# Kernel tuning notes

Measured on AMD Instinct MI355X. Metric: run time of the kernel, lower is better.

The kernel has to match this reference:

```python
import jax, jax.numpy as jnp
import numpy as np

LN_EPS = 1e-5   # torch nn.LayerNorm default
R_EPS = 1e-8    # eps used in log(R.clamp(min=eps))


def layernorm(x, g, b):
    mu = jnp.mean(x, axis=-1, keepdims=True)
    var = jnp.var(x, axis=-1, keepdims=True)
    return (x - mu) * jax.lax.rsqrt(var + LN_EPS) * g + b


def setup_inputs() -> dict:
    S, B, C, h, w, d = 4, 1, 128, 10, 10, 10
    nL = 2  # num_layers
    key = jax.random.key(0)
    ks = jax.random.split(key, 20)
    std = 0.02
    inp = {
        "z": jax.random.normal(ks[0], (S, B, C, h, w, d), jnp.float32),
        "r": jax.random.uniform(ks[1], (S,), jnp.float32, 0.1, 1.0),
        "seq_embed": std * jax.random.normal(ks[2], (S, C), jnp.float32),
        # per-layer attention params, stacked on leading layer axis
        "Wq": std * jax.random.normal(ks[3], (nL, C, C), jnp.float32),
        "Wk": std * jax.random.normal(ks[4], (nL, C, C), jnp.float32),
        "Wv": std * jax.random.normal(ks[5], (nL, C, C), jnp.float32),
        "Wp": std * jax.random.normal(ks[6], (nL, C, C), jnp.float32),
        "beta": jnp.ones((nL,), jnp.float32),
        "ln1_g": jnp.ones((nL, C), jnp.float32),
        "ln1_b": jnp.zeros((nL, C), jnp.float32),
        # FFN params
        "ffn_w1": std * jax.random.normal(ks[7], (C, 4 * C), jnp.float32),
        "ffn_b1": jnp.zeros((4 * C,), jnp.float32),
        "ffn_w2": std * jax.random.normal(ks[8], (4 * C, C), jnp.float32),
        "ffn_b2": jnp.zeros((C,), jnp.float32),
        "ln2_g": jnp.ones((C,), jnp.float32),
        "ln2_b": jnp.zeros((C,), jnp.float32),
    }
    return inp


def _forward(z, r, seq_embed, Wq, Wk, Wv, Wp, beta, ln1_g, ln1_b,
             ffn_w1, ffn_b1, ffn_w2, ffn_b2, ln2_g, ln2_b):
    S, B, C, h, w, d = z.shape
    N = h * w * d
    L = S * N
    nL, _, _ = Wq.shape
    H = 8
    Dh = C // H
    scale = Dh ** (-0.5)

    # tokenize: [S,B,C,h,w,d] -> [B, S*N, C] with per-sequence embedding added
    tokens = z.reshape(S, B, C, N).transpose(1, 0, 3, 2)      # [B,S,N,C]
    tokens = tokens + seq_embed[None, :, None, :]
    tokens = tokens.reshape(B, L, C)

    # reliability bias: log(clamp(outer(r_tok, r_tok), eps))  [L,L]
    r_tok = jnp.repeat(r, N)                                   # [L]
    log_R = jnp.log(jnp.clip(r_tok[:, None] * r_tok[None, :], R_EPS, None))

    for l in range(nL):
        residual = tokens
        Q = (tokens @ Wq[l]).reshape(B, L, H, Dh)
        K = (tokens @ Wk[l]).reshape(B, L, H, Dh)
        V = (tokens @ Wv[l]).reshape(B, L, H, Dh)
        attn = jnp.einsum('bihd,bjhd->bhij', Q, K) * scale     # [B,H,L,L]
        attn = attn + beta[l] * log_R[None, None]
        attn = jax.nn.softmax(attn, axis=-1)
        out = jnp.einsum('bhij,bjhd->bihd', attn, V).reshape(B, L, C)
        out = out @ Wp[l]
        tokens = layernorm(out + residual, ln1_g[l], ln1_b[l])

    # FFN (exact GELU, matching torch nn.GELU default) + residual + LN
    hdn = jax.nn.gelu(tokens @ ffn_w1 + ffn_b1, approximate=False)
    tokens = layernorm((hdn @ ffn_w2 + ffn_b2) + tokens, ln2_g, ln2_b)

    # de-tokenize: [B,L,C] -> [B, S*C, h, w, d]
    tokens = tokens.reshape(B, S, N, C).transpose(0, 1, 3, 2)  # [B,S,C,N]
    return tokens.reshape(B, S * C, h, w, d)


def reference(z, r, seq_embed, Wq, Wk, Wv, Wp, beta, ln1_g, ln1_b,
              ffn_w1, ffn_b1, ffn_w2, ffn_b2, ln2_g, ln2_b):
    return _forward(z, r, seq_embed, Wq, Wk, Wv, Wp, beta, ln1_g, ln1_b,
                    ffn_w1, ffn_b1, ffn_w2, ffn_b2, ln2_g, ln2_b)
```

## Files before the change

### kernel.cpp

```cpp
#include <hip/hip_runtime.h>
#include <hip/hip_bf16.h>
#include <math.h>

#define LL 4000
#define CC 128
#define NN 1000
#define NLAYER 2
#define KSPLIT 4
#define SCLOG2 0.36067376022224085f
#define KROW 20
#define VROW 36

typedef __attribute__((ext_vector_type(4))) short bf16x4;
typedef __attribute__((ext_vector_type(8))) short short8;
typedef __attribute__((ext_vector_type(4))) float f32x4;
typedef __attribute__((ext_vector_type(2))) unsigned int u32x2;

__device__ __forceinline__ short bf16rne(float f) {
    return __builtin_bit_cast(short, __float2bfloat16(f));
}
__device__ __forceinline__ float bf16tof(short s) {
    return __builtin_bit_cast(float, (unsigned)((unsigned short)s) << 16);
}

__device__ __forceinline__ bf16x4 pack4(const float* p) {
    unsigned w01 = __builtin_amdgcn_perm(__builtin_bit_cast(unsigned, p[1]),
                                         __builtin_bit_cast(unsigned, p[0]),
                                         0x07060302u);
    unsigned w23 = __builtin_amdgcn_perm(__builtin_bit_cast(unsigned, p[3]),
                                         __builtin_bit_cast(unsigned, p[2]),
                                         0x07060302u);
    u32x2 w = {w01, w23};
    return __builtin_bit_cast(bf16x4, w);
}

__global__ void tokenize_kernel(const float* __restrict__ z,
                                const float* __restrict__ se,
                                float* __restrict__ tok,
                                short* __restrict__ tokb) {
    __shared__ float tl[32][33];
    const int s  = blockIdx.z;
    const int c0 = blockIdx.y * 32;
    const int n0 = blockIdx.x * 32;
    const int tx = threadIdx.x & 31, ty = threadIdx.x >> 5;
    #pragma unroll
    for (int i = 0; i < 4; ++i) {
        int n = n0 + tx;
        if (n < NN) tl[ty * 4 + i][tx] = z[((size_t)s * CC + c0 + ty * 4 + i) * NN + n];
    }
    __syncthreads();
    #pragma unroll
    for (int i = 0; i < 4; ++i) {
        int n = n0 + ty * 4 + i;
        if (n < NN) {
            int c = c0 + tx;
            float v = tl[tx][ty * 4 + i] + se[s * CC + c];
            size_t o = ((size_t)(s * NN + n)) * CC + c;
            tok[o] = v;
            tokb[o] = bf16rne(v);
        }
    }
}

__global__ void detok_kernel(const float* __restrict__ tok,
                             float* __restrict__ out) {
    __shared__ float tl[32][33];
    const int s  = blockIdx.z;
    const int c0 = blockIdx.y * 32;
    const int n0 = blockIdx.x * 32;
    const int tx = threadIdx.x & 31, ty = threadIdx.x >> 5;
    #pragma unroll
    for (int i = 0; i < 4; ++i) {
        int n = n0 + ty * 4 + i;
        if (n < NN) tl[ty * 4 + i][tx] = tok[((size_t)(s * NN + n)) * CC + c0 + tx];
    }
    __syncthreads();
    #pragma unroll
    for (int i = 0; i < 4; ++i) {
        int n = n0 + tx;
        if (n < NN) out[((size_t)s * CC + c0 + ty * 4 + i) * NN + n] = tl[tx][ty * 4 + i];
    }
}

__global__ void prep_weights(const float* __restrict__ Wq, const float* __restrict__ Wk,
                             const float* __restrict__ Wv, const float* __restrict__ Wp,
                             const float* __restrict__ w1, const float* __restrict__ w2,
                             const float* __restrict__ r, const float* __restrict__ beta,
                             short* __restrict__ wt8, short* __restrict__ w1t,
                             short* __restrict__ w2t, float* __restrict__ kbw) {
    int idx = blockIdx.x * blockDim.x + threadIdx.x;
    if (idx < 8 * 16384) {
        int m = idx >> 14, i = idx & 16383;
        int n = i >> 7, k = i & 127;
        const float* src = (m < 2) ? Wq + (size_t)m * 16384
                         : (m < 4) ? Wk + (size_t)(m - 2) * 16384
                         : (m < 6) ? Wv + (size_t)(m - 4) * 16384
                                   : Wp + (size_t)(m - 6) * 16384;
        wt8[idx] = bf16rne(src[k * 128 + n]);
    } else if (idx < 8 * 16384 + 65536) {
        int i = idx - 8 * 16384;
        int n = i >> 7, k = i & 127;
        w1t[i] = bf16rne(w1[(size_t)k * 512 + n]);
    } else if (idx < 8 * 16384 + 2 * 65536) {
        int i = idx - 8 * 16384 - 65536;
        int n = i >> 9, k = i & 511;
        w2t[i] = bf16rne(w2[(size_t)k * 128 + n]);
    } else if (idx < 8 * 16384 + 2 * 65536 + NLAYER * KSPLIT) {
        int i = idx - (8 * 16384 + 2 * 65536);
        int l = i / KSPLIT, zz = i - l * KSPLIT;
        kbw[i] = exp2f(beta[l] * __log2f(r[zz]));
    }
}

__device__ __forceinline__ void gemm_body(
        const short* __restrict__ A, const short* __restrict__ Wt,
        const float* __restrict__ bias, void* __restrict__ outp,
        int M, int K, int N, int flags, int row0, int col0) {
    __shared__ short Al[16][136];
    __shared__ short Wl[128][136];
    const int tid = threadIdx.x;
    const int lane = tid & 63;
    const int w = tid >> 6;
    const int lq = lane & 15, g = lane >> 4;

    f32x4 acc[2] = {{0.f,0.f,0.f,0.f},{0.f,0.f,0.f,0.f}};

    for (int kc = 0; kc < K; kc += 128) {
        {
            int r = tid >> 4, c = (tid & 15) * 8;
            *(short8*)&Al[r][c] = *(const short8*)(A + (size_t)(row0 + r) * K + kc + c);
        }
        {
            int c = (tid & 15) * 8;
            int nb = tid >> 4;
            #pragma unroll
            for (int i = 0; i < 8; ++i) {
                int n = nb + i * 16;
                *(short8*)&Wl[n][c] = *(const short8*)(Wt + (size_t)(col0 + n) * K + kc + c);
            }
        }
        __syncthreads();
        bf16x4 af[8];
        #pragma unroll
        for (int ks = 0; ks < 8; ++ks)
            af[ks] = *(const bf16x4*)&Al[lq][ks * 16 + g * 4];
        #pragma unroll
        for (int ct = 0; ct < 2; ++ct) {
            int n = (w * 2 + ct) * 16 + lq;
            #pragma unroll
            for (int ks = 0; ks < 8; ++ks) {
                bf16x4 bfr = *(const bf16x4*)&Wl[n][ks * 16 + g * 4];
                acc[ct] = __builtin_amdgcn_mfma_f32_16x16x16bf16_1k(af[ks], bfr, acc[ct], 0, 0, 0);
            }
        }
        __syncthreads();
    }
    #pragma unroll
    for (int ct = 0; ct < 2; ++ct) {
        int col = col0 + (w * 2 + ct) * 16 + lq;
        float bv = bias ? bias[col] : 0.f;
        float v[4];
        #pragma unroll
        for (int r = 0; r < 4; ++r) {
            v[r] = acc[ct][r] + bv;
            if (flags & 2) v[r] = 0.5f * v[r] * (1.f + erff(v[r] * 0.70710678118654752f));
            if (flags & 8) v[r] *= SCLOG2;
        }
        if (flags & 4) {
            bf16x4 res = {bf16rne(v[0]), bf16rne(v[1]), bf16rne(v[2]), bf16rne(v[3])};
            *(bf16x4*)((short*)outp + (size_t)col * M + row0 + g * 4) = res;
        } else if (flags & 16) {
            #pragma unroll
            for (int r = 0; r < 4; ++r)
                ((short*)outp)[((size_t)(col >> 4) * M + (row0 + g * 4 + r)) * 16 + (col & 15)] = bf16rne(v[r]);
        } else if (flags & 1) {
            #pragma unroll
            for (int r = 0; r < 4; ++r)
                ((short*)outp)[(size_t)(row0 + g * 4 + r) * N + col] = bf16rne(v[r]);
        } else {
            #pragma unroll
            for (int r = 0; r < 4; ++r)
                ((float*)outp)[(size_t)(row0 + g * 4 + r) * N + col] = v[r];
        }
    }
}

__global__ __launch_bounds__(256) void mfma_gemm(
        const short* __restrict__ A, const short* __restrict__ Wt,
        const float* __restrict__ bias, void* __restrict__ outp,
        int M, int K, int N, int flags) {
    gemm_body(A, Wt, bias, outp, M, K, N, flags,
              blockIdx.x * 16, blockIdx.y * 128);
}

__global__ __launch_bounds__(256) void mfma_gemm3(
        const short* __restrict__ A,
        const short* __restrict__ W0, const short* __restrict__ W1,
        const short* __restrict__ W2,
        short* __restrict__ o0, short* __restrict__ o1, short* __restrict__ o2,
        int M, int K, int N) {
    const short* Wt = (blockIdx.z == 0) ? W0 : (blockIdx.z == 1) ? W1 : W2;
    short* o = (blockIdx.z == 0) ? o0 : (blockIdx.z == 1) ? o1 : o2;
    int flags = (blockIdx.z == 0) ? (1 | 8) : (blockIdx.z == 1) ? 16 : 4;
    gemm_body(A, Wt, nullptr, o, M, K, N, flags, blockIdx.x * 16, 0);
}

__global__ __launch_bounds__(256) void mfma_gemm_ln(
        const short* __restrict__ A, const short* __restrict__ Wt,
        const float* __restrict__ bias, const float* __restrict__ resid,
        const float* __restrict__ gam, const float* __restrict__ bet,
        float* __restrict__ outf, short* __restrict__ outb,
        int M, int K) {
    __shared__ short Al[16][136];
    __shared__ short Wl[128][136];
    __shared__ float sL[4][4][4], s2L[4][4][4];
    const int tid = threadIdx.x;
    const int lane = tid & 63;
    const int w = tid >> 6;
    const int lq = lane & 15, g = lane >> 4;
    const int row0 = blockIdx.x * 16;

    f32x4 acc[2] = {{0.f,0.f,0.f,0.f},{0.f,0.f,0.f,0.f}};

    for (int kc = 0; kc < K; kc += 128) {
        {
            int r = tid >> 4, c = (tid & 15) * 8;
            *(short8*)&Al[r][c] = *(const short8*)(A + (size_t)(row0 + r) * K + kc + c);
        }
        {
            int c = (tid & 15) * 8;
            int nb = tid >> 4;
            #pragma unroll
            for (int i = 0; i < 8; ++i) {
                int n = nb + i * 16;
                *(short8*)&Wl[n][c] = *(const short8*)(Wt + (size_t)n * K + kc + c);
            }
        }
        __syncthreads();
        bf16x4 af[8];
        #pragma unroll
        for (int ks = 0; ks < 8; ++ks)
            af[ks] = *(const bf16x4*)&Al[lq][ks * 16 + g * 4];
        #pragma unroll
        for (int ct = 0; ct < 2; ++ct) {
            int n = (w * 2 + ct) * 16 + lq;
            #pragma unroll
            for (int ks = 0; ks < 8; ++ks) {
                bf16x4 bfr = *(const bf16x4*)&Wl[n][ks * 16 + g * 4];
                acc[ct] = __builtin_amdgcn_mfma_f32_16x16x16bf16_1k(af[ks], bfr, acc[ct], 0, 0, 0);
            }
        }
        __syncthreads();
    }

    float v[2][4];
    int cols[2] = {(w * 2) * 16 + lq, (w * 2 + 1) * 16 + lq};
    #pragma unroll
    for (int ct = 0; ct < 2; ++ct) {
        float bv = bias ? bias[cols[ct]] : 0.f;
        #pragma unroll
        for (int r = 0; r < 4; ++r)
            v[ct][r] = acc[ct][r] + bv +
                       resid[(size_t)(row0 + g * 4 + r) * CC + cols[ct]];
    }
    float sr[4], s2r[4];
    #pragma unroll
    for (int r = 0; r < 4; ++r) {
        sr[r]  = v[0][r] + v[1][r];
        s2r[r] = v[0][r] * v[0][r] + v[1][r] * v[1][r];
    }
    #pragma unroll
    for (int off = 1; off < 16; off <<= 1) {
        #pragma unroll
        for (int r = 0; r < 4; ++r) {
            sr[r]  += __shfl_xor(sr[r],  off);
            s2r[r] += __shfl_xor(s2r[r], off);
        }
    }
    if (lq == 0) {
        #pragma unroll
        for (int r = 0; r < 4; ++r) { sL[w][g][r] = sr[r]; s2L[w][g][r] = s2r[r]; }
    }
    __syncthreads();
    #pragma unroll
    for (int r = 0; r < 4; ++r) {
        float s = 0.f, s2 = 0.f;
        #pragma unroll
        for (int ww = 0; ww < 4; ++ww) { s += sL[ww][g][r]; s2 += s2L[ww][g][r]; }
        float mu = s * (1.f / CC);
        float var = s2 * (1.f / CC) - mu * mu;
        float rstd = rsqrtf(var + 1e-5f);
        size_t rowoff = (size_t)(row0 + g * 4 + r) * CC;
        #pragma unroll
        for (int ct = 0; ct < 2; ++ct) {
            float y = (v[ct][r] - mu) * rstd * gam[cols[ct]] + bet[cols[ct]];
            outf[rowoff + cols[ct]] = y;
            outb[rowoff + cols[ct]] = bf16rne(y);
        }
    }
}

__global__ __launch_bounds__(256) void attn_mfma_kernel(
        const short* __restrict__ Qb, const short* __restrict__ Kh,
        const short* __restrict__ Vt, const float* __restrict__ kbw,
        short* __restrict__ pob, float* __restrict__ pl) {
    __shared__ short Kl[2][32][KROW];
    __shared__ short Vl[2][16][VROW];
    const int tid  = threadIdx.x;
    const int lane = tid & 63;
    const int wv   = tid >> 6;
    const int lq = lane & 15;
    const int g  = lane >> 4;
    const int h  = blockIdx.y;
    const int z  = blockIdx.z;
    const int qt = blockIdx.x * 4 + wv;
    const int q0 = qt * 16;
    const int hd0 = h * 16;
    const int kbase = z * NN;
    const bool qvalid = qt < LL / 16;

    bf16x4 qf = {0, 0, 0, 0};
    if (qvalid) qf = *(const bf16x4*)(Qb + (size_t)(q0 + lq) * CC + hd0 + 4 * g);

    const short onev = (lq == 0) ? (short)0x3F80 : (short)0;
    const bf16x4 af1 = {onev, onev, onev, onev};

    const short* kgp = Kh + ((size_t)h * LL + kbase) * 16 + tid * 2;
    const short* vgp = Vt + (size_t)(hd0 + (tid >> 4)) * LL + kbase + (tid & 15) * 2;
    short* kwp = &Kl[0][0][0] + (tid >> 3) * KROW + (tid & 7) * 2;
    short* vwp = &Vl[0][0][0] + (tid >> 4) * VROW + (tid & 15) * 2;
    const int kbufstride = 32 * KROW;
    const int vbufstride = 16 * VROW;

    f32x4 o  = {0.f, 0.f, 0.f, 0.f};
    f32x4 ps = {0.f, 0.f, 0.f, 0.f};

    {
        unsigned kd = *(const unsigned*)kgp;
        unsigned vd = *(const unsigned*)vgp;
        *(unsigned*)kwp = kd;
        *(unsigned*)vwp = vd;
    }
    unsigned kdA = *(const unsigned*)(kgp + (size_t)32 * 16);
    unsigned vdA = *(const unsigned*)(vgp + 32);
    __syncthreads();

    for (int t = 0; t < 31; ++t) {
        unsigned kdB, vdB;
        if (t < 30) {
            kdB = *(const unsigned*)(kgp + (size_t)(t + 2) * 32 * 16);
            vdB = *(const unsigned*)(vgp + (t + 2) * 32);
        }

        {
            const short* kb = &Kl[t & 1][0][0];
            const short* vb = &Vl[t & 1][0][0];
            bf16x4 K0 = *(const bf16x4*)(kb + lq * KROW + 4 * g);
            bf16x4 K1 = *(const bf16x4*)(kb + (16 + lq) * KROW + 4 * g);
            bf16x4 V0 = *(const bf16x4*)(vb + lq * VROW + 4 * g);
            bf16x4 V1 = *(const bf16x4*)(vb + lq * VROW + 16 + 4 * g);
            const f32x4 zz = {0.f, 0.f, 0.f, 0.f};
            f32x4 s0 = __builtin_amdgcn_mfma_f32_16x16x16bf16_1k(K0, qf, zz, 0, 0, 0);
            f32x4 s1 = __builtin_amdgcn_mfma_f32_16x16x16bf16_1k(K1, qf, zz, 0, 0, 0);
            float p0[4], p1[4];
            #pragma unroll
            for (int r = 0; r < 4; ++r) {
                p0[r] = __builtin_amdgcn_exp2f(s0[r]);
                p1[r] = __builtin_amdgcn_exp2f(s1[r]);
            }
            bf16x4 pt0 = pack4(p0);
            bf16x4 pt1 = pack4(p1);
            o  = __builtin_amdgcn_mfma_f32_16x16x16bf16_1k(V0, pt0, o, 0, 0, 0);
            o  = __builtin_amdgcn_mfma_f32_16x16x16bf16_1k(V1, pt1, o, 0, 0, 0);
            ps = __builtin_amdgcn_mfma_f32_16x16x16bf16_1k(af1, pt0, ps, 0, 0, 0);
            ps = __builtin_amdgcn_mfma_f32_16x16x16bf16_1k(af1, pt1, ps, 0, 0, 0);
        }

        const int nb = (t + 1) & 1;
        *(unsigned*)(kwp + nb * kbufstride) = kdA;
        *(unsigned*)(vwp + nb * vbufstride) = vdA;
        __syncthreads();
        if (t < 30) { kdA = kdB; vdA = vdB; }
    }

    {
        const short* kb = &Kl[1][0][0];
        const short* vb = &Vl[1][0][0];
        bf16x4 K0 = *(const bf16x4*)(kb + lq * KROW + 4 * g);
        bf16x4 V0 = *(const bf16x4*)(vb + lq * VROW + 4 * g);
        if (g >= 2) V0 = (bf16x4){0, 0, 0, 0};
        const f32x4 zz = {0.f, 0.f, 0.f, 0.f};
        f32x4 s0 = __builtin_amdgcn_mfma_f32_16x16x16bf16_1k(K0, qf, zz, 0, 0, 0);
        float p0[4];
        #pragma unroll
        for (int r = 0; r < 4; ++r)
            p0[r] = (g < 2) ? __builtin_amdgcn_exp2f(s0[r]) : 0.f;
        bf16x4 pt0 = pack4(p0);
        o  = __builtin_amdgcn_mfma_f32_16x16x16bf16_1k(V0, pt0, o, 0, 0, 0);
        ps = __builtin_amdgcn_mfma_f32_16x16x16bf16_1k(af1, pt0, ps, 0, 0, 0);
    }

    if (qvalid) {
        const float wz = kbw[z];
        bf16x4 ow = {bf16rne(o[0] * wz), bf16rne(o[1] * wz),
                     bf16rne(o[2] * wz), bf16rne(o[3] * wz)};
        *(bf16x4*)(pob + (size_t)z * LL * CC + (size_t)(q0 + lq) * CC + hd0 + 4 * g) = ow;
        if (g == 0) pl[(z * 8 + h) * LL + q0 + lq] = ps[0] * wz;
    }
}

__global__ void attn_combine(const short* __restrict__ pob,
                             const float* __restrict__ pl,
                             short* __restrict__ attb) {
    int i = blockIdx.x * blockDim.x + threadIdx.x;
    if (i >= LL * CC / 4) return;
    int q  = i >> 5;
    int c0 = (i & 31) * 4;
    int h  = c0 >> 4;
    size_t off = (size_t)q * CC + c0;
    float o0 = 0.f, o1 = 0.f, o2 = 0.f, o3 = 0.f;
    float l = 0.f;
    #pragma unroll
    for (int zz = 0; zz < KSPLIT; ++zz) {
        bf16x4 t = *(const bf16x4*)(pob + (size_t)zz * LL * CC + off);
        o0 += bf16tof(t[0]); o1 += bf16tof(t[1]);
        o2 += bf16tof(t[2]); o3 += bf16tof(t[3]);
        l += pl[(zz * 8 + h) * LL + q];
    }
    float inv = 1.f / l;
    bf16x4 res = {bf16rne(o0 * inv), bf16rne(o1 * inv),
                  bf16rne(o2 * inv), bf16rne(o3 * inv)};
    *(bf16x4*)(attb + off) = res;
}

extern "C" void kernel_launch(void* const* d_in, const int* in_sizes, int n_in,
                              void* d_out, int out_size, void* d_ws, size_t ws_size,
                              hipStream_t stream) {
    const float* z    = (const float*)d_in[0];
    const float* r    = (const float*)d_in[1];
    const float* se   = (const float*)d_in[2];
    const float* Wq   = (const float*)d_in[3];
    const float* Wk   = (const float*)d_in[4];
    const float* Wv   = (const float*)d_in[5];
    const float* Wp   = (const float*)d_in[6];
    const float* beta = (const float*)d_in[7];
    const float* ln1g = (const float*)d_in[8];
    const float* ln1b = (const float*)d_in[9];
    const float* w1   = (const float*)d_in[10];
    const float* b1   = (const float*)d_in[11];
    const float* w2   = (const float*)d_in[12];
    const float* b2   = (const float*)d_in[13];
    const float* ln2g = (const float*)d_in[14];
    const float* ln2b = (const float*)d_in[15];
    float* out = (float*)d_out;

    float* ws   = (float*)d_ws;
    float* tok  = ws;
    float* kbw  = tok + LL * CC;
    float* pl   = kbw + 8;
    short* pob  = (short*)(pl + KSPLIT * 8 * LL);
    short* hdn  = pob;
    short* tokb = pob + (size_t)KSPLIT * LL * CC;
    short* attb = tokb + LL * CC;
    short* Qb   = attb + LL * CC;
    short* Kh   = Qb   + LL * CC;
    short* Vt   = Kh   + LL * CC + 1024;
    short* wt8  = Vt   + LL * CC + 1024;
    short* w1t  = wt8  + 8 * 16384;
    short* w2t  = w1t  + 65536;

    prep_weights<<<1025, 256, 0, stream>>>(Wq, Wk, Wv, Wp, w1, w2, r, beta,
                                           wt8, w1t, w2t, kbw);
    tokenize_kernel<<<dim3(32, 4, 4), 256, 0, stream>>>(z, se, tok, tokb);

    for (int l = 0; l < NLAYER; ++l) {
        const short* wqt = wt8 + (size_t)(0 * 2 + l) * 16384;
        const short* wkt = wt8 + (size_t)(1 * 2 + l) * 16384;
        const short* wvt = wt8 + (size_t)(2 * 2 + l) * 16384;
        const short* wpt = wt8 + (size_t)(3 * 2 + l) * 16384;
        mfma_gemm3<<<dim3(LL / 16, 1, 3), 256, 0, stream>>>(
            tokb, wqt, wkt, wvt, Qb, Kh, Vt, LL, CC, CC);
        attn_mfma_kernel<<<dim3((LL / 16 + 3) / 4, 8, KSPLIT), 256, 0, stream>>>(
            Qb, Kh, Vt, kbw + l * KSPLIT, pob, pl);
        attn_combine<<<(LL * CC / 4 + 255) / 256, 256, 0, stream>>>(pob, pl, attb);
        mfma_gemm_ln<<<LL / 16, 256, 0, stream>>>(
            attb, wpt, nullptr, tok, ln1g + l * CC, ln1b + l * CC,
            tok, tokb, LL, CC);
    }

    mfma_gemm<<<dim3(LL / 16, 4), 256, 0, stream>>>(tokb, w1t, b1, hdn, LL, CC, 4 * CC, 1 | 2);
    mfma_gemm_ln<<<LL / 16, 256, 0, stream>>>(
        hdn, w2t, b2, tok, ln2g, ln2b, tok, tokb, LL, 4 * CC);

    detok_kernel<<<dim3(32, 4, 4), 256, 0, stream>>>(tok, out);
}
```

Measured before the change: 104.1 us.

## Fuse split-K attention combine into projection GEMM+LN; two query tiles per wave

Removes the separate attn_combine kernel by merging the KSPLIT partial outputs and denominators directly into the A-tile load of a new projection GEMM+LayerNorm kernel, which drops a launch and a round trip of the attention output through global memory. The attention kernel now processes two 16-query tiles per wave, so each K/V tile staged in shared memory serves twice as many queries, at the cost of more registers and half as many blocks.

```diff
diff --git a/kernel.cpp b/kernel.cpp
--- a/kernel.cpp
+++ b/kernel.cpp
@@ -300,6 +300,111 @@
     }
 }
 
+__global__ __launch_bounds__(256) void mfma_gemm_ln_cmb(
+        const short* __restrict__ pob, const float* __restrict__ pl,
+        const short* __restrict__ Wt, const float* __restrict__ resid,
+        const float* __restrict__ gam, const float* __restrict__ bet,
+        float* __restrict__ outf, short* __restrict__ outb) {
+    __shared__ short Al[16][136];
+    __shared__ short Wl[128][136];
+    __shared__ float sL[4][4][4], s2L[4][4][4];
+    const int tid = threadIdx.x;
+    const int lane = tid & 63;
+    const int w = tid >> 6;
+    const int lq = lane & 15, g = lane >> 4;
+    const int row0 = blockIdx.x * 16;
+
+    {
+        int r = tid >> 4, c0 = (tid & 15) * 8;
+        int row = row0 + r;
+        int h = c0 >> 4;
+        float a8[8] = {0.f,0.f,0.f,0.f,0.f,0.f,0.f,0.f};
+        float den = 0.f;
+        #pragma unroll
+        for (int zz = 0; zz < KSPLIT; ++zz) {
+            short8 t = *(const short8*)(pob + (size_t)zz * LL * CC + (size_t)row * CC + c0);
+            #pragma unroll
+            for (int j = 0; j < 8; ++j) a8[j] += bf16tof(t[j]);
+            den += pl[(zz * 8 + h) * LL + row];
+        }
+        float inv = 1.f / den;
+        short8 packed;
+        #pragma unroll
+        for (int j = 0; j < 8; ++j) packed[j] = bf16rne(a8[j] * inv);
+        *(short8*)&Al[r][c0] = packed;
+    }
+    {
+        int c = (tid & 15) * 8;
+        int nb = tid >> 4;
+        #pragma unroll
+        for (int i = 0; i < 8; ++i) {
+            int n = nb + i * 16;
+            *(short8*)&Wl[n][c] = *(const short8*)(Wt + (size_t)n * CC + c);
+        }
+    }
+    __syncthreads();
+
+    f32x4 acc[2] = {{0.f,0.f,0.f,0.f},{0.f,0.f,0.f,0.f}};
+    bf16x4 af[8];
+    #pragma unroll
+    for (int ks = 0; ks < 8; ++ks)
+        af[ks] = *(const bf16x4*)&Al[lq][ks * 16 + g * 4];
+    #pragma unroll
+    for (int ct = 0; ct < 2; ++ct) {
+        int n = (w * 2 + ct) * 16 + lq;
+        #pragma unroll
+        for (int ks = 0; ks < 8; ++ks) {
+            bf16x4 bfr = *(const bf16x4*)&Wl[n][ks * 16 + g * 4];
+            acc[ct] = __builtin_amdgcn_mfma_f32_16x16x16bf16_1k(af[ks], bfr, acc[ct], 0, 0, 0);
+        }
+    }
+
+    float v[2][4];
+    int cols[2] = {(w * 2) * 16 + lq, (w * 2 + 1) * 16 + lq};
+    #pragma unroll
+    for (int ct = 0; ct < 2; ++ct) {
+        #pragma unroll
+        for (int r = 0; r < 4; ++r)
+            v[ct][r] = acc[ct][r] +
+                       resid[(size_t)(row0 + g * 4 + r) * CC + cols[ct]];
+    }
+    float sr[4], s2r[4];
+    #pragma unroll
+    for (int r = 0; r < 4; ++r) {
+        sr[r]  = v[0][r] + v[1][r];
+        s2r[r] = v[0][r] * v[0][r] + v[1][r] * v[1][r];
+    }
+    #pragma unroll
+    for (int off = 1; off < 16; off <<= 1) {
+        #pragma unroll
+        for (int r = 0; r < 4; ++r) {
+            sr[r]  += __shfl_xor(sr[r],  off);
+            s2r[r] += __shfl_xor(s2r[r], off);
+        }
+    }
+    if (lq == 0) {
+        #pragma unroll
+        for (int r = 0; r < 4; ++r) { sL[w][g][r] = sr[r]; s2L[w][g][r] = s2r[r]; }
+    }
+    __syncthreads();
+    #pragma unroll
+    for (int r = 0; r < 4; ++r) {
+        float s = 0.f, s2 = 0.f;
+        #pragma unroll
+        for (int ww = 0; ww < 4; ++ww) { s += sL[ww][g][r]; s2 += s2L[ww][g][r]; }
+        float mu = s * (1.f / CC);
+        float var = s2 * (1.f / CC) - mu * mu;
+        float rstd = rsqrtf(var + 1e-5f);
+        size_t rowoff = (size_t)(row0 + g * 4 + r) * CC;
+        #pragma unroll
+        for (int ct = 0; ct < 2; ++ct) {
+            float y = (v[ct][r] - mu) * rstd * gam[cols[ct]] + bet[cols[ct]];
+            outf[rowoff + cols[ct]] = y;
+            outb[rowoff + cols[ct]] = bf16rne(y);
+        }
+    }
+}
+
 __global__ __launch_bounds__(256) void attn_mfma_kernel(
         const short* __restrict__ Qb, const short* __restrict__ Kh,
         const short* __restrict__ Vt, const float* __restrict__ kbw,
@@ -313,14 +418,16 @@
     const int g  = lane >> 4;
     const int h  = blockIdx.y;
     const int z  = blockIdx.z;
-    const int qt = blockIdx.x * 4 + wv;
-    const int q0 = qt * 16;
+    const int qtA = blockIdx.x * 8 + wv * 2;
+    const int qtB = qtA + 1;
+    const bool qvA = qtA < LL / 16;
+    const bool qvB = qtB < LL / 16;
     const int hd0 = h * 16;
     const int kbase = z * NN;
-    const bool qvalid = qt < LL / 16;
-
-    bf16x4 qf = {0, 0, 0, 0};
-    if (qvalid) qf = *(const bf16x4*)(Qb + (size_t)(q0 + lq) * CC + hd0 + 4 * g);
+
+    bf16x4 qfA = {0, 0, 0, 0}, qfB = {0, 0, 0, 0};
+    if (qvA) qfA = *(const bf16x4*)(Qb + (size_t)(qtA * 16 + lq) * CC + hd0 + 4 * g);
+    if (qvB) qfB = *(const bf16x4*)(Qb + (size_t)(qtB * 16 + lq) * CC + hd0 + 4 * g);
 
     const short onev = (lq == 0) ? (short)0x3F80 : (short)0;
     const bf16x4 af1 = {onev, onev, onev, onev};
@@ -332,8 +439,8 @@
     const int kbufstride = 32 * KROW;
     const int vbufstride = 16 * VROW;
 
-    f32x4 o  = {0.f, 0.f, 0.f, 0.f};
-    f32x4 ps = {0.f, 0.f, 0.f, 0.f};
+    f32x4 oA  = {0.f, 0.f, 0.f, 0.f}, oB  = {0.f, 0.f, 0.f, 0.f};
+    f32x4 psA = {0.f, 0.f, 0.f, 0.f}, psB = {0.f, 0.f, 0.f, 0.f};
 
     {
         unsigned kd = *(const unsigned*)kgp;
@@ -360,20 +467,28 @@
             bf16x4 V0 = *(const bf16x4*)(vb + lq * VROW + 4 * g);
             bf16x4 V1 = *(const bf16x4*)(vb + lq * VROW + 16 + 4 * g);
             const f32x4 zz = {0.f, 0.f, 0.f, 0.f};
-            f32x4 s0 = __builtin_amdgcn_mfma_f32_16x16x16bf16_1k(K0, qf, zz, 0, 0, 0);
-            f32x4 s1 = __builtin_amdgcn_mfma_f32_16x16x16bf16_1k(K1, qf, zz, 0, 0, 0);
-            float p0[4], p1[4];
+            f32x4 sA0 = __builtin_amdgcn_mfma_f32_16x16x16bf16_1k(K0, qfA, zz, 0, 0, 0);
+            f32x4 sA1 = __builtin_amdgcn_mfma_f32_16x16x16bf16_1k(K1, qfA, zz, 0, 0, 0);
+            f32x4 sB0 = __builtin_amdgcn_mfma_f32_16x16x16bf16_1k(K0, qfB, zz, 0, 0, 0);
+            f32x4 sB1 = __builtin_amdgcn_mfma_f32_16x16x16bf16_1k(K1, qfB, zz, 0, 0, 0);
+            float pA0[4], pA1[4], pB0[4], pB1[4];
             #pragma unroll
             for (int r = 0; r < 4; ++r) {
-                p0[r] = __builtin_amdgcn_exp2f(s0[r]);
-                p1[r] = __builtin_amdgcn_exp2f(s1[r]);
+                pA0[r] = __builtin_amdgcn_exp2f(sA0[r]);
+                pA1[r] = __builtin_amdgcn_exp2f(sA1[r]);
+                pB0[r] = __builtin_amdgcn_exp2f(sB0[r]);
+                pB1[r] = __builtin_amdgcn_exp2f(sB1[r]);
             }
-            bf16x4 pt0 = pack4(p0);
-            bf16x4 pt1 = pack4(p1);
-            o  = __builtin_amdgcn_mfma_f32_16x16x16bf16_1k(V0, pt0, o, 0, 0, 0);
-            o  = __builtin_amdgcn_mfma_f32_16x16x16bf16_1k(V1, pt1, o, 0, 0, 0);
-            ps = __builtin_amdgcn_mfma_f32_16x16x16bf16_1k(af1, pt0, ps, 0, 0, 0);
-            ps = __builtin_amdgcn_mfma_f32_16x16x16bf16_1k(af1, pt1, ps, 0, 0, 0);
+            bf16x4 ptA0 = pack4(pA0), ptA1 = pack4(pA1);
+            bf16x4 ptB0 = pack4(pB0), ptB1 = pack4(pB1);
+            oA  = __builtin_amdgcn_mfma_f32_16x16x16bf16_1k(V0, ptA0, oA, 0, 0, 0);
+            oA  = __builtin_amdgcn_mfma_f32_16x16x16bf16_1k(V1, ptA1, oA, 0, 0, 0);
+            oB  = __builtin_amdgcn_mfma_f32_16x16x16bf16_1k(V0, ptB0, oB, 0, 0, 0);
+            oB  = __builtin_amdgcn_mfma_f32_16x16x16bf16_1k(V1, ptB1, oB, 0, 0, 0);
+            psA = __builtin_amdgcn_mfma_f32_16x16x16bf16_1k(af1, ptA0, psA, 0, 0, 0);
+            psA = __builtin_amdgcn_mfma_f32_16x16x16bf16_1k(af1, ptA1, psA, 0, 0, 0);
+            psB = __builtin_amdgcn_mfma_f32_16x16x16bf16_1k(af1, ptB0, psB, 0, 0, 0);
+            psB = __builtin_amdgcn_mfma_f32_16x16x16bf16_1k(af1, ptB1, psB, 0, 0, 0);
         }
 
         const int nb = (t + 1) & 1;
@@ -390,47 +505,34 @@
         bf16x4 V0 = *(const bf16x4*)(vb + lq * VROW + 4 * g);
         if (g >= 2) V0 = (bf16x4){0, 0, 0, 0};
         const f32x4 zz = {0.f, 0.f, 0.f, 0.f};
-        f32x4 s0 = __builtin_amdgcn_mfma_f32_16x16x16bf16_1k(K0, qf, zz, 0, 0, 0);
-        float p0[4];
-        #pragma unroll
-        for (int r = 0; r < 4; ++r)
-            p0[r] = (g < 2) ? __builtin_amdgcn_exp2f(s0[r]) : 0.f;
-        bf16x4 pt0 = pack4(p0);
-        o  = __builtin_amdgcn_mfma_f32_16x16x16bf16_1k(V0, pt0, o, 0, 0, 0);
-        ps = __builtin_amdgcn_mfma_f32_16x16x16bf16_1k(af1, pt0, ps, 0, 0, 0);
-    }
-
-    if (qvalid) {
-        const float wz = kbw[z];
-        bf16x4 ow = {bf16rne(o[0] * wz), bf16rne(o[1] * wz),
-                     bf16rne(o[2] * wz), bf16rne(o[3] * wz)};
-        *(bf16x4*)(pob + (size_t)z * LL * CC + (size_t)(q0 + lq) * CC + hd0 + 4 * g) = ow;
-        if (g == 0) pl[(z * 8 + h) * LL + q0 + lq] = ps[0] * wz;
-    }
-}
-
-__global__ void attn_combine(const short* __restrict__ pob,
-                             const float* __restrict__ pl,
-                             short* __restrict__ attb) {
-    int i = blockIdx.x * blockDim.x + threadIdx.x;
-    if (i >= LL * CC / 4) return;
-    int q  = i >> 5;
-    int c0 = (i & 31) * 4;
-    int h  = c0 >> 4;
-    size_t off = (size_t)q * CC + c0;
-    float o0 = 0.f, o1 = 0.f, o2 = 0.f, o3 = 0.f;
-    float l = 0.f;
-    #pragma unroll
-    for (int zz = 0; zz < KSPLIT; ++zz) {
-        bf16x4 t = *(const bf16x4*)(pob + (size_t)zz * LL * CC + off);
-        o0 += bf16tof(t[0]); o1 += bf16tof(t[1]);
-        o2 += bf16tof(t[2]); o3 += bf16tof(t[3]);
-        l += pl[(zz * 8 + h) * LL + q];
-    }
-    float inv = 1.f / l;
-    bf16x4 res = {bf16rne(o0 * inv), bf16rne(o1 * inv),
-                  bf16rne(o2 * inv), bf16rne(o3 * inv)};
-    *(bf16x4*)(attb + off) = res;
+        f32x4 sA0 = __builtin_amdgcn_mfma_f32_16x16x16bf16_1k(K0, qfA, zz, 0, 0, 0);
+        f32x4 sB0 = __builtin_amdgcn_mfma_f32_16x16x16bf16_1k(K0, qfB, zz, 0, 0, 0);
+        float pA0[4], pB0[4];
+        #pragma unroll
+        for (int r = 0; r < 4; ++r) {
+            pA0[r] = (g < 2) ? __builtin_amdgcn_exp2f(sA0[r]) : 0.f;
+            pB0[r] = (g < 2) ? __builtin_amdgcn_exp2f(sB0[r]) : 0.f;
+        }
+        bf16x4 ptA0 = pack4(pA0), ptB0 = pack4(pB0);
+        oA  = __builtin_amdgcn_mfma_f32_16x16x16bf16_1k(V0, ptA0, oA, 0, 0, 0);
+        oB  = __builtin_amdgcn_mfma_f32_16x16x16bf16_1k(V0, ptB0, oB, 0, 0, 0);
+        psA = __builtin_amdgcn_mfma_f32_16x16x16bf16_1k(af1, ptA0, psA, 0, 0, 0);
+        psB = __builtin_amdgcn_mfma_f32_16x16x16bf16_1k(af1, ptB0, psB, 0, 0, 0);
+    }
+
+    const float wz = kbw[z];
+    if (qvA) {
+        bf16x4 ow = {bf16rne(oA[0] * wz), bf16rne(oA[1] * wz),
+                     bf16rne(oA[2] * wz), bf16rne(oA[3] * wz)};
+        *(bf16x4*)(pob + (size_t)z * LL * CC + (size_t)(qtA * 16 + lq) * CC + hd0 + 4 * g) = ow;
+        if (g == 0) pl[(z * 8 + h) * LL + qtA * 16 + lq] = psA[0] * wz;
+    }
+    if (qvB) {
+        bf16x4 ow = {bf16rne(oB[0] * wz), bf16rne(oB[1] * wz),
+                     bf16rne(oB[2] * wz), bf16rne(oB[3] * wz)};
+        *(bf16x4*)(pob + (size_t)z * LL * CC + (size_t)(qtB * 16 + lq) * CC + hd0 + 4 * g) = ow;
+        if (g == 0) pl[(z * 8 + h) * LL + qtB * 16 + lq] = psB[0] * wz;
+    }
 }
 
 extern "C" void kernel_launch(void* const* d_in, const int* in_sizes, int n_in,
@@ -461,8 +563,7 @@
     short* pob  = (short*)(pl + KSPLIT * 8 * LL);
     short* hdn  = pob;
     short* tokb = pob + (size_t)KSPLIT * LL * CC;
-    short* attb = tokb + LL * CC;
-    short* Qb   = attb + LL * CC;
+    short* Qb   = tokb + LL * CC;
     short* Kh   = Qb   + LL * CC;
     short* Vt   = Kh   + LL * CC + 1024;
     short* wt8  = Vt   + LL * CC + 1024;
@@ -480,12 +581,10 @@
         const short* wpt = wt8 + (size_t)(3 * 2 + l) * 16384;
         mfma_gemm3<<<dim3(LL / 16, 1, 3), 256, 0, stream>>>(
             tokb, wqt, wkt, wvt, Qb, Kh, Vt, LL, CC, CC);
-        attn_mfma_kernel<<<dim3((LL / 16 + 3) / 4, 8, KSPLIT), 256, 0, stream>>>(
+        attn_mfma_kernel<<<dim3((LL / 16 + 7) / 8, 8, KSPLIT), 256, 0, stream>>>(
             Qb, Kh, Vt, kbw + l * KSPLIT, pob, pl);
-        attn_combine<<<(LL * CC / 4 + 255) / 256, 256, 0, stream>>>(pob, pl, attb);
-        mfma_gemm_ln<<<LL / 16, 256, 0, stream>>>(
-            attb, wpt, nullptr, tok, ln1g + l * CC, ln1b + l * CC,
-            tok, tokb, LL, CC);
+        mfma_gemm_ln_cmb<<<LL / 16, 256, 0, stream>>>(
+            pob, pl, wpt, tok, ln1g + l * CC, ln1b + l * CC, tok, tokb);
     }
 
     mfma_gemm<<<dim3(LL / 16, 4), 256, 0, stream>>>(tokb, w1t, b1, hdn, LL, CC, 4 * CC, 1 | 2);
```

Result: faster. 100.2 us (-3.8%).
